# Performance work log

Measured on AMD Instinct MI355X. Metric: run time of the kernel, lower is better.

The kernel has to match this reference:

```python
import jax, jax.numpy as jnp
import numpy as np

B, S, T = 512, 1024, 48  # batch, seq_len, num_tags


def setup_inputs() -> dict:
    key = jax.random.key(0)
    k1, k2, k3, k4, k5, k6 = jax.random.split(key, 6)
    emissions = jax.random.normal(k1, (B, S, T), dtype=jnp.float32)
    tags = jax.random.randint(k2, (B, S), 0, T)
    lengths = jax.random.randint(k3, (B,), 1, S + 1)
    mask = jnp.arange(S)[None, :] < lengths[:, None]  # contiguous prefix mask, bool
    # learned parameters (nn.Parameter zeros init in the module; use small random here)
    start_transitions = 0.01 * jax.random.normal(k4, (T,), dtype=jnp.float32)
    end_transitions = 0.01 * jax.random.normal(k5, (T,), dtype=jnp.float32)
    transitions = 0.01 * jax.random.normal(k6, (T, T), dtype=jnp.float32)
    return {
        "emissions": emissions,
        "tags": tags,
        "mask": mask,
        "start_transitions": start_transitions,
        "end_transitions": end_transitions,
        "transitions": transitions,
    }


def _log_partition(emissions, mask, start_transitions, end_transitions, transitions):
    # score[b, i] = log-sum over paths ending in tag i (note: this repo indexes
    # transitions[i, j] with j = previous tag inside the partition recursion).
    score0 = start_transitions[None, :] + emissions[:, 0]  # (B, T)

    def step(score, xs):
        emit_t, mask_t = xs  # (B, T), (B,)
        # score_t[b, i] = logsumexp_j(score[b, j] + transitions[i, j]) + emit_t[b, i]
        score_t = jax.nn.logsumexp(score[:, None, :] + transitions[None, :, :], axis=2) + emit_t
        score = jnp.where(mask_t[:, None], score_t, score)
        return score, None

    em = jnp.swapaxes(emissions[:, 1:], 0, 1)  # (S-1, B, T)
    mk = jnp.swapaxes(mask[:, 1:], 0, 1)       # (S-1, B)
    score, _ = jax.lax.scan(step, score0, (em, mk))
    return jax.nn.logsumexp(score + end_transitions[None, :], axis=1)  # (B,)


def _score_sentence(emissions, tags, mask, start_transitions, end_transitions, transitions):
    Bb = emissions.shape[0]
    bidx = jnp.arange(Bb)
    maskf = mask.astype(emissions.dtype)
    score = start_transitions[tags[:, 0]] + emissions[bidx, 0, tags[:, 0]]  # (B,)
    trans_sc = transitions[tags[:, :-1], tags[:, 1:]]  # (B, S-1)
    emit_sc = jnp.take_along_axis(emissions, tags[:, :, None], axis=2)[..., 0]  # (B, S)
    score = score + jnp.sum((trans_sc + emit_sc[:, 1:]) * maskf[:, 1:], axis=1)
    last_idx = jnp.sum(mask.astype(jnp.int32), axis=1) - 1  # (B,)
    last_tags = jnp.take_along_axis(tags, last_idx[:, None], axis=1)[:, 0]
    return score + end_transitions[last_tags]


def reference(emissions, tags, mask, start_transitions, end_transitions, transitions):
    log_denominator = _log_partition(emissions, mask, start_transitions, end_transitions, transitions)
    log_numerator = _score_sentence(emissions, tags, mask, start_transitions, end_transitions, transitions)
    return jnp.mean(log_denominator - log_numerator)
```

## Files before the change

### kernel.cpp

```cpp
#include <hip/hip_runtime.h>

#define BB 512
#define SS 1024
#define TT 48
#define GG 16
#define CK 8
#define NSLOT 5

typedef __attribute__((ext_vector_type(8))) short short8;
typedef __attribute__((ext_vector_type(4))) float float4v;
typedef unsigned uint2v __attribute__((ext_vector_type(2)));

__device__ __forceinline__ unsigned short f2bf(float x) {
    unsigned u = __float_as_uint(x);
    u += 0x7FFFu + ((u >> 16) & 1u);
    return (unsigned short)(u >> 16);
}
__device__ __forceinline__ unsigned pk2bf(float lo, float hi) {
#if __has_builtin(__builtin_amdgcn_cvt_pk_bf16_f32)
    typedef __bf16 bf16x2 __attribute__((ext_vector_type(2)));
    union { bf16x2 v; unsigned u; } cv;
    cv.v = __builtin_amdgcn_cvt_pk_bf16_f32(lo, hi);
    return cv.u;
#else
    return __builtin_amdgcn_perm(__float_as_uint(hi) + 0x8000u,
                                 __float_as_uint(lo) + 0x8000u, 0x07060302u);
#endif
}
__device__ __forceinline__ float bflo(unsigned u) { return __uint_as_float(u << 16); }
__device__ __forceinline__ float bfhi(unsigned u) { return __uint_as_float(u & 0xFFFF0000u); }
__device__ __forceinline__ float wave_sum(float v) {
#pragma unroll
    for (int off = 32; off >= 1; off >>= 1) v += __shfl_xor(v, off, 64);
    return v;
}
__device__ __forceinline__ int wave_sum_i(int v) {
#pragma unroll
    for (int off = 32; off >= 1; off >>= 1) v += __shfl_xor(v, off, 64);
    return v;
}
__device__ __forceinline__ float xgrp_max(float m) {
#if __has_builtin(__builtin_amdgcn_permlane16_swap) && __has_builtin(__builtin_amdgcn_permlane32_swap)
    uint2v a = __builtin_amdgcn_permlane16_swap(__float_as_uint(m), __float_as_uint(m), false, false);
    m = fmaxf(__uint_as_float(a[0]), __uint_as_float(a[1]));
    uint2v b = __builtin_amdgcn_permlane32_swap(__float_as_uint(m), __float_as_uint(m), false, false);
    m = fmaxf(__uint_as_float(b[0]), __uint_as_float(b[1]));
#else
    m = fmaxf(m, __shfl_xor(m, 16, 64));
    m = fmaxf(m, __shfl_xor(m, 32, 64));
#endif
    return m;
}
__device__ __forceinline__ float xgrp_sum(float m) {
#if __has_builtin(__builtin_amdgcn_permlane16_swap) && __has_builtin(__builtin_amdgcn_permlane32_swap)
    uint2v a = __builtin_amdgcn_permlane16_swap(__float_as_uint(m), __float_as_uint(m), false, false);
    m = __uint_as_float(a[0]) + __uint_as_float(a[1]);
    uint2v b = __builtin_amdgcn_permlane32_swap(__float_as_uint(m), __float_as_uint(m), false, false);
    m = __uint_as_float(b[0]) + __uint_as_float(b[1]);
#else
    m += __shfl_xor(m, 16, 64);
    m += __shfl_xor(m, 32, 64);
#endif
    return m;
}

__global__ __launch_bounds__(256)
void crf_numer(const float* __restrict__ em, const int* __restrict__ tags,
               const int* __restrict__ mask, const float* __restrict__ start_tr,
               const float* __restrict__ end_tr, const float* __restrict__ trans,
               float* __restrict__ numer, int* __restrict__ lenArr) {
    const int b = blockIdx.x, tid = threadIdx.x;
    const float* emb = em + (size_t)b * SS * TT;
    const int* tg = tags + (size_t)b * SS;
    const int* mk = mask + (size_t)b * SS;
    const int s0 = tid * 4;
    const int4 t4 = *(const int4*)(tg + s0);
    const int4 m4 = *(const int4*)(mk + s0);
    const int tprev = (tid == 0) ? 0 : tg[s0 - 1];
    int cnt = (m4.x != 0) + (m4.y != 0) + (m4.z != 0) + (m4.w != 0);
    float ns = 0.f;
    if (tid > 0 && m4.x) ns += trans[tprev * TT + t4.x] + emb[(size_t)s0 * TT + t4.x];
    if (m4.y) ns += trans[t4.x * TT + t4.y] + emb[(size_t)(s0 + 1) * TT + t4.y];
    if (m4.z) ns += trans[t4.y * TT + t4.z] + emb[(size_t)(s0 + 2) * TT + t4.z];
    if (m4.w) ns += trans[t4.z * TT + t4.w] + emb[(size_t)(s0 + 3) * TT + t4.w];
    float wsum = wave_sum(ns);
    int wcnt = wave_sum_i(cnt);
    __shared__ float sf[4]; __shared__ int si[4];
    if ((tid & 63) == 0) { sf[tid >> 6] = wsum; si[tid >> 6] = wcnt; }
    __syncthreads();
    if (tid == 0) {
        float tot = sf[0] + sf[1] + sf[2] + sf[3];
        int L = si[0] + si[1] + si[2] + si[3];
        int t0 = tg[0];
        tot += start_tr[t0] + emb[t0] + end_tr[tg[L - 1]];
        numer[b] = tot;
        lenArr[b] = L;
    }
}

__global__ __launch_bounds__(320, 1)
void crf_fwd(const float* __restrict__ em, const float* __restrict__ start_tr,
             const float* __restrict__ end_tr, const float* __restrict__ trans,
             const int* __restrict__ lenArr, float* __restrict__ denomArr) {
    __shared__ uint2 ring[NSLOT * CK * 3 * 64];

    const int tid = threadIdx.x;
    const int wave = tid >> 6, lane = tid & 63;
    const int wgbase = blockIdx.x * GG;

    if (wave == 0) {
        __builtin_amdgcn_s_setprio(1);
        const int n = lane & 15, q = lane >> 4;
        const int bb = wgbase + n;

        short8 afr[3][2];
#pragma unroll
        for (int mt = 0; mt < 3; ++mt) {
            const int so = mt * 16 + n;
#pragma unroll
            for (int kt = 0; kt < 2; ++kt) {
                short8 a;
#pragma unroll
                for (int i = 0; i < 8; ++i) {
                    int si_;
                    if (kt == 0) si_ = (i < 4) ? (q * 4 + i) : (16 + q * 4 + (i - 4));
                    else         si_ = (i < 4) ? (32 + q * 4 + i) : -1;
                    a[i] = (si_ >= 0) ? (short)f2bf(__expf(trans[so * TT + si_])) : (short)0;
                }
                afr[mt][kt] = a;
            }
        }

        const float* em0 = em + (size_t)bb * SS * TT + q * 4;
        float p[3][4];
#pragma unroll
        for (int mt = 0; mt < 3; ++mt) {
            float4 v = *(const float4*)(em0 + mt * 16);
            int sb = mt * 16 + q * 4;
            p[mt][0] = __expf(start_tr[sb + 0] + v.x);
            p[mt][1] = __expf(start_tr[sb + 1] + v.y);
            p[mt][2] = __expf(start_tr[sb + 2] + v.z);
            p[mt][3] = __expf(start_tr[sb + 3] + v.w);
        }

        const int len = lenArr[bb];
        int Lmax = len;
#pragma unroll
        for (int off = 1; off < 64; off <<= 1) {
            int o = __shfl_xor(Lmax, off, 64);
            Lmax = Lmax > o ? Lmax : o;
        }
        const int P = (Lmax + 6) >> 3;

        float dc[3][4];
#pragma unroll
        for (int mt = 0; mt < 3; ++mt)
#pragma unroll
            for (int r = 0; r < 4; ++r) dc[mt][r] = 0.f;
        float lcap = 0.f, logscale = 0.f;
        const float4v Z = {0.f, 0.f, 0.f, 0.f};

        for (int pp = -3; pp < P; ++pp) {
            if (pp >= 0) {
                const uint2* rp = &ring[(pp % NSLOT) * (CK * 3 * 64) + lane];
                uint2 c0 = rp[0], c1 = rp[64], c2v = rp[128];
#pragma unroll
                for (int u = 0; u < 8; ++u) {
                    union { short8 v; unsigned w[4]; } B0, B1;
                    B0.w[0] = pk2bf(p[0][0], p[0][1]); B0.w[1] = pk2bf(p[0][2], p[0][3]);
                    B0.w[2] = pk2bf(p[1][0], p[1][1]); B0.w[3] = pk2bf(p[1][2], p[1][3]);
                    B1.w[0] = pk2bf(p[2][0], p[2][1]); B1.w[1] = pk2bf(p[2][2], p[2][3]);
                    B1.w[2] = 0u; B1.w[3] = 0u;
                    float4v A0a = __builtin_amdgcn_mfma_f32_16x16x32_bf16(afr[0][0], B0.v, Z, 0, 0, 0);
                    float4v A1a = __builtin_amdgcn_mfma_f32_16x16x32_bf16(afr[1][0], B0.v, Z, 0, 0, 0);
                    float4v A2a = __builtin_amdgcn_mfma_f32_16x16x32_bf16(afr[2][0], B0.v, Z, 0, 0, 0);
                    float4v A0b = __builtin_amdgcn_mfma_f32_16x16x32_bf16(afr[0][1], B1.v, Z, 0, 0, 0);
                    float4v A1b = __builtin_amdgcn_mfma_f32_16x16x32_bf16(afr[1][1], B1.v, Z, 0, 0, 0);
                    float4v A2b = __builtin_amdgcn_mfma_f32_16x16x32_bf16(afr[2][1], B1.v, Z, 0, 0, 0);
                    uint2 n0, n1, n2;
                    if (u < 7) {
                        n0 = rp[(u + 1) * 192];
                        n1 = rp[(u + 1) * 192 + 64];
                        n2 = rp[(u + 1) * 192 + 128];
                    }
                    float e00 = bflo(c0.x),  e01 = bfhi(c0.x),  e02 = bflo(c0.y),  e03 = bfhi(c0.y);
                    float e10 = bflo(c1.x),  e11 = bfhi(c1.x),  e12 = bflo(c1.y),  e13 = bfhi(c1.y);
                    float e20 = bflo(c2v.x), e21 = bfhi(c2v.x), e22 = bflo(c2v.y), e23 = bfhi(c2v.y);
                    bool cc = (len == 8 * pp + u + 1);
#pragma unroll
                    for (int mt = 0; mt < 3; ++mt)
#pragma unroll
                        for (int r = 0; r < 4; ++r) dc[mt][r] = cc ? p[mt][r] : dc[mt][r];
                    lcap = cc ? logscale : lcap;
                    p[0][0] = (A0a[0] + A0b[0]) * e00; p[0][1] = (A0a[1] + A0b[1]) * e01;
                    p[0][2] = (A0a[2] + A0b[2]) * e02; p[0][3] = (A0a[3] + A0b[3]) * e03;
                    p[1][0] = (A1a[0] + A1b[0]) * e10; p[1][1] = (A1a[1] + A1b[1]) * e11;
                    p[1][2] = (A1a[2] + A1b[2]) * e12; p[1][3] = (A1a[3] + A1b[3]) * e13;
                    p[2][0] = (A2a[0] + A2b[0]) * e20; p[2][1] = (A2a[1] + A2b[1]) * e21;
                    p[2][2] = (A2a[2] + A2b[2]) * e22; p[2][3] = (A2a[3] + A2b[3]) * e23;
                    c0 = n0; c1 = n1; c2v = n2;
                    if (u == 7) {
                        float m = fmaxf(fmaxf(p[0][0], p[0][1]), fmaxf(p[0][2], p[0][3]));
                        m = fmaxf(m, fmaxf(fmaxf(p[1][0], p[1][1]), fmaxf(p[1][2], p[1][3])));
                        m = fmaxf(m, fmaxf(fmaxf(p[2][0], p[2][1]), fmaxf(p[2][2], p[2][3])));
                        m = xgrp_max(m);
                        m = fmaxf(m, 1e-30f);
                        logscale += __logf(m);
                        float rm = __builtin_amdgcn_rcpf(m);
#pragma unroll
                        for (int mt = 0; mt < 3; ++mt)
#pragma unroll
                            for (int r = 0; r < 4; ++r) p[mt][r] *= rm;
                    }
                }
            }
            __builtin_amdgcn_s_barrier();
        }
        {
            bool cc = (len == 8 * P + 1);
#pragma unroll
            for (int mt = 0; mt < 3; ++mt)
#pragma unroll
                for (int r = 0; r < 4; ++r) dc[mt][r] = cc ? p[mt][r] : dc[mt][r];
            lcap = cc ? logscale : lcap;
        }

        float pe = 0.f;
#pragma unroll
        for (int mt = 0; mt < 3; ++mt) {
            int sb = mt * 16 + q * 4;
            pe = fmaf(dc[mt][0], __expf(end_tr[sb + 0]), pe);
            pe = fmaf(dc[mt][1], __expf(end_tr[sb + 1]), pe);
            pe = fmaf(dc[mt][2], __expf(end_tr[sb + 2]), pe);
            pe = fmaf(dc[mt][3], __expf(end_tr[sb + 3]), pe);
        }
        pe = xgrp_sum(pe);
        if (lane < 16) denomArr[bb] = lcap + __logf(pe);

    } else {
        const int T = (wave - 1) >> 1;
        const int sub = (wave - 1) & 1;
        const int nb = lane & 15, q4 = lane >> 4;
        const int bb = wgbase + nb;
        const int len_v = lenArr[bb];
        int Lmax = len_v;
#pragma unroll
        for (int off = 1; off < 64; off <<= 1) {
            int o = __shfl_xor(Lmax, off, 64);
            Lmax = Lmax > o ? Lmax : o;
        }
        const int P = (Lmax + 6) >> 3;

        const float* emP = em + (size_t)bb * SS * TT + q4 * 4;
        float4 buf[12];

        for (int pp = -3; pp < P; ++pp) {
            int cv = pp + 1;
            if (cv >= 0 && cv < P && (cv & 1) == T) {
                uint2* wp = &ring[(cv % NSLOT) * (CK * 3 * 64) + lane];
#pragma unroll
                for (int k = 0; k < 12; ++k) {
                    const int i = sub * 12 + k, u = i / 3, j = i % 3;
                    int t = 1 + 8 * cv + u;
                    bool live = t < len_v;
                    float4 v = buf[k];
                    unsigned ox = pk2bf(__expf(v.x), __expf(v.y));
                    unsigned oy = pk2bf(__expf(v.z), __expf(v.w));
                    uint2 o;
                    o.x = live ? ox : 0u;
                    o.y = live ? oy : 0u;
                    wp[u * 192 + j * 64] = o;
                }
            }
            int ci = pp + 3;
            if (ci < P && (ci & 1) == T) {
#pragma unroll
                for (int k = 0; k < 12; ++k) {
                    const int i = sub * 12 + k, u = i / 3, j = i % 3;
                    int t = 1 + 8 * ci + u; t = t < SS ? t : SS - 1;
                    buf[k] = *(const float4*)(emP + (size_t)t * TT + j * 16);
                }
            }
            __builtin_amdgcn_s_waitcnt(0xC07F);
            __builtin_amdgcn_s_barrier();
        }
    }
}

__global__ __launch_bounds__(64)
void crf_reduce(const float* __restrict__ denom, const float* __restrict__ numer,
                float* __restrict__ out) {
    int lane = threadIdx.x;
    float s = 0.f;
    for (int i = lane; i < BB; i += 64) s += denom[i] - numer[i];
    s = wave_sum(s);
    if (lane == 0) out[0] = s * (1.0f / (float)BB);
}

extern "C" void kernel_launch(void* const* d_in, const int* in_sizes, int n_in,
                              void* d_out, int out_size, void* d_ws, size_t ws_size,
                              hipStream_t stream) {
    const float* emissions = (const float*)d_in[0];
    const int*   tags      = (const int*)d_in[1];
    const int*   mask      = (const int*)d_in[2];
    const float* start_tr  = (const float*)d_in[3];
    const float* end_tr    = (const float*)d_in[4];
    const float* trans     = (const float*)d_in[5];

    char* ws = (char*)d_ws;
    float* denom = (float*)ws;
    float* numer = (float*)(ws + 2048);
    int*   lenA  = (int*)(ws + 4096);

    crf_numer<<<BB, 256, 0, stream>>>(emissions, tags, mask, start_tr, end_tr,
                                      trans, numer, lenA);
    crf_fwd<<<BB / GG, 320, 0, stream>>>(emissions, start_tr, end_tr, trans,
                                         lenA, denom);
    crf_reduce<<<1, 64, 0, stream>>>(denom, numer, (float*)d_out);
}
```

Measured before the change: 339.0 us.

## Interleave two 16-sequence batches per compute wave and store fp32 emission ring

Each workgroup now handles 32 sequences. The MFMA wave runs two independent forward recursions, A and B, interleaving their MFMAs to hide dependency latency, and chains the two K-halves through the accumulator instead of adding them afterwards. The LDS ring now holds fp32 exp(emissions) instead of bf16, which removes the unpack work. Producer waves drop from four to three, staggered over three chunks, and the capture bookkeeping is skipped unless a ballot says some sequence ends in that chunk. Halving the grid to 16 workgroups cuts GPU-wide parallelism, and fp32 staging doubles LDS traffic.

```diff
diff --git a/kernel.cpp b/kernel.cpp
--- a/kernel.cpp
+++ b/kernel.cpp
@@ -3,9 +3,9 @@
 #define BB 512
 #define SS 1024
 #define TT 48
-#define GG 16
+#define GG 32
 #define CK 8
-#define NSLOT 5
+#define NSLOT 3
 
 typedef __attribute__((ext_vector_type(8))) short short8;
 typedef __attribute__((ext_vector_type(4))) float float4v;
@@ -27,8 +27,6 @@
                                  __float_as_uint(lo) + 0x8000u, 0x07060302u);
 #endif
 }
-__device__ __forceinline__ float bflo(unsigned u) { return __uint_as_float(u << 16); }
-__device__ __forceinline__ float bfhi(unsigned u) { return __uint_as_float(u & 0xFFFF0000u); }
 __device__ __forceinline__ float wave_sum(float v) {
 #pragma unroll
     for (int off = 32; off >= 1; off >>= 1) v += __shfl_xor(v, off, 64);
@@ -98,20 +96,21 @@
     }
 }
 
-__global__ __launch_bounds__(320, 1)
+__global__ __launch_bounds__(256, 1)
 void crf_fwd(const float* __restrict__ em, const float* __restrict__ start_tr,
              const float* __restrict__ end_tr, const float* __restrict__ trans,
              const int* __restrict__ lenArr, float* __restrict__ denomArr) {
-    __shared__ uint2 ring[NSLOT * CK * 3 * 64];
+    __shared__ float4v ring[NSLOT * CK * 3 * 2 * 64];
 
     const int tid = threadIdx.x;
     const int wave = tid >> 6, lane = tid & 63;
     const int wgbase = blockIdx.x * GG;
+    const float4v Zv = {0.f, 0.f, 0.f, 0.f};
 
     if (wave == 0) {
         __builtin_amdgcn_s_setprio(1);
         const int n = lane & 15, q = lane >> 4;
-        const int bb = wgbase + n;
+        const int bbA = wgbase + n, bbB = wgbase + 16 + n;
 
         short8 afr[3][2];
 #pragma unroll
@@ -131,20 +130,24 @@
             }
         }
 
-        const float* em0 = em + (size_t)bb * SS * TT + q * 4;
-        float p[3][4];
+        const float* em0A = em + (size_t)bbA * SS * TT + q * 4;
+        const float* em0B = em + (size_t)bbB * SS * TT + q * 4;
+        float4v pA[3], pB[3];
 #pragma unroll
         for (int mt = 0; mt < 3; ++mt) {
-            float4 v = *(const float4*)(em0 + mt * 16);
-            int sb = mt * 16 + q * 4;
-            p[mt][0] = __expf(start_tr[sb + 0] + v.x);
-            p[mt][1] = __expf(start_tr[sb + 1] + v.y);
-            p[mt][2] = __expf(start_tr[sb + 2] + v.z);
-            p[mt][3] = __expf(start_tr[sb + 3] + v.w);
-        }
-
-        const int len = lenArr[bb];
-        int Lmax = len;
+            float4v vA = *(const float4v*)(em0A + mt * 16);
+            float4v vB = *(const float4v*)(em0B + mt * 16);
+            const int sb = mt * 16 + q * 4;
+#pragma unroll
+            for (int r = 0; r < 4; ++r) {
+                float st = start_tr[sb + r];
+                pA[mt][r] = __expf(st + vA[r]);
+                pB[mt][r] = __expf(st + vB[r]);
+            }
+        }
+
+        const int lenA = lenArr[bbA], lenB = lenArr[bbB];
+        int Lmax = lenA > lenB ? lenA : lenB;
 #pragma unroll
         for (int off = 1; off < 64; off <<= 1) {
             int o = __shfl_xor(Lmax, off, 64);
@@ -152,98 +155,115 @@
         }
         const int P = (Lmax + 6) >> 3;
 
-        float dc[3][4];
-#pragma unroll
-        for (int mt = 0; mt < 3; ++mt)
-#pragma unroll
-            for (int r = 0; r < 4; ++r) dc[mt][r] = 0.f;
-        float lcap = 0.f, logscale = 0.f;
-        const float4v Z = {0.f, 0.f, 0.f, 0.f};
+        float4v dcA[3], dcB[3];
+        {
+            const bool c0A = (lenA == 1), c0B = (lenB == 1);
+#pragma unroll
+            for (int mt = 0; mt < 3; ++mt) {
+                dcA[mt] = c0A ? pA[mt] : Zv;
+                dcB[mt] = c0B ? pB[mt] : Zv;
+            }
+        }
+        float lcapA = 0.f, lcapB = 0.f, lsA = 0.f, lsB = 0.f;
 
         for (int pp = -3; pp < P; ++pp) {
             if (pp >= 0) {
-                const uint2* rp = &ring[(pp % NSLOT) * (CK * 3 * 64) + lane];
-                uint2 c0 = rp[0], c1 = rp[64], c2v = rp[128];
+                const float4v* rp = ring + (size_t)(pp % NSLOT) * (CK * 3 * 2 * 64) + lane;
+                float4v cA0 = rp[0],  cA1 = rp[128], cA2 = rp[256];
+                float4v cB0 = rp[64], cB1 = rp[192], cB2 = rp[320];
+                const int lo = 8 * pp + 2, hi = 8 * pp + 9;
+                const bool any =
+                    __ballot(((lenA >= lo) & (lenA <= hi)) | ((lenB >= lo) & (lenB <= hi))) != 0ull;
 #pragma unroll
                 for (int u = 0; u < 8; ++u) {
-                    union { short8 v; unsigned w[4]; } B0, B1;
-                    B0.w[0] = pk2bf(p[0][0], p[0][1]); B0.w[1] = pk2bf(p[0][2], p[0][3]);
-                    B0.w[2] = pk2bf(p[1][0], p[1][1]); B0.w[3] = pk2bf(p[1][2], p[1][3]);
-                    B1.w[0] = pk2bf(p[2][0], p[2][1]); B1.w[1] = pk2bf(p[2][2], p[2][3]);
-                    B1.w[2] = 0u; B1.w[3] = 0u;
-                    float4v A0a = __builtin_amdgcn_mfma_f32_16x16x32_bf16(afr[0][0], B0.v, Z, 0, 0, 0);
-                    float4v A1a = __builtin_amdgcn_mfma_f32_16x16x32_bf16(afr[1][0], B0.v, Z, 0, 0, 0);
-                    float4v A2a = __builtin_amdgcn_mfma_f32_16x16x32_bf16(afr[2][0], B0.v, Z, 0, 0, 0);
-                    float4v A0b = __builtin_amdgcn_mfma_f32_16x16x32_bf16(afr[0][1], B1.v, Z, 0, 0, 0);
-                    float4v A1b = __builtin_amdgcn_mfma_f32_16x16x32_bf16(afr[1][1], B1.v, Z, 0, 0, 0);
-                    float4v A2b = __builtin_amdgcn_mfma_f32_16x16x32_bf16(afr[2][1], B1.v, Z, 0, 0, 0);
-                    uint2 n0, n1, n2;
+                    union { short8 v; unsigned w[4]; } BA0, BA1, BB0, BB1;
+                    BA0.w[0] = pk2bf(pA[0][0], pA[0][1]); BA0.w[1] = pk2bf(pA[0][2], pA[0][3]);
+                    BA0.w[2] = pk2bf(pA[1][0], pA[1][1]); BA0.w[3] = pk2bf(pA[1][2], pA[1][3]);
+                    BA1.w[0] = pk2bf(pA[2][0], pA[2][1]); BA1.w[1] = pk2bf(pA[2][2], pA[2][3]);
+                    BA1.w[2] = 0u; BA1.w[3] = 0u;
+                    BB0.w[0] = pk2bf(pB[0][0], pB[0][1]); BB0.w[1] = pk2bf(pB[0][2], pB[0][3]);
+                    BB0.w[2] = pk2bf(pB[1][0], pB[1][1]); BB0.w[3] = pk2bf(pB[1][2], pB[1][3]);
+                    BB1.w[0] = pk2bf(pB[2][0], pB[2][1]); BB1.w[1] = pk2bf(pB[2][2], pB[2][3]);
+                    BB1.w[2] = 0u; BB1.w[3] = 0u;
+                    float4v rA0 = __builtin_amdgcn_mfma_f32_16x16x32_bf16(afr[0][0], BA0.v, Zv, 0, 0, 0);
+                    float4v rB0 = __builtin_amdgcn_mfma_f32_16x16x32_bf16(afr[0][0], BB0.v, Zv, 0, 0, 0);
+                    float4v rA1 = __builtin_amdgcn_mfma_f32_16x16x32_bf16(afr[1][0], BA0.v, Zv, 0, 0, 0);
+                    float4v rB1 = __builtin_amdgcn_mfma_f32_16x16x32_bf16(afr[1][0], BB0.v, Zv, 0, 0, 0);
+                    float4v rA2 = __builtin_amdgcn_mfma_f32_16x16x32_bf16(afr[2][0], BA0.v, Zv, 0, 0, 0);
+                    float4v rB2 = __builtin_amdgcn_mfma_f32_16x16x32_bf16(afr[2][0], BB0.v, Zv, 0, 0, 0);
+                    rA0 = __builtin_amdgcn_mfma_f32_16x16x32_bf16(afr[0][1], BA1.v, rA0, 0, 0, 0);
+                    rB0 = __builtin_amdgcn_mfma_f32_16x16x32_bf16(afr[0][1], BB1.v, rB0, 0, 0, 0);
+                    rA1 = __builtin_amdgcn_mfma_f32_16x16x32_bf16(afr[1][1], BA1.v, rA1, 0, 0, 0);
+                    rB1 = __builtin_amdgcn_mfma_f32_16x16x32_bf16(afr[1][1], BB1.v, rB1, 0, 0, 0);
+                    rA2 = __builtin_amdgcn_mfma_f32_16x16x32_bf16(afr[2][1], BA1.v, rA2, 0, 0, 0);
+                    rB2 = __builtin_amdgcn_mfma_f32_16x16x32_bf16(afr[2][1], BB1.v, rB2, 0, 0, 0);
+                    float4v nA0, nA1, nA2, nB0, nB1, nB2;
                     if (u < 7) {
-                        n0 = rp[(u + 1) * 192];
-                        n1 = rp[(u + 1) * 192 + 64];
-                        n2 = rp[(u + 1) * 192 + 128];
+                        nA0 = rp[(u + 1) * 384];       nA1 = rp[(u + 1) * 384 + 128];
+                        nA2 = rp[(u + 1) * 384 + 256];
+                        nB0 = rp[(u + 1) * 384 + 64];  nB1 = rp[(u + 1) * 384 + 192];
+                        nB2 = rp[(u + 1) * 384 + 320];
                     }
-                    float e00 = bflo(c0.x),  e01 = bfhi(c0.x),  e02 = bflo(c0.y),  e03 = bfhi(c0.y);
-                    float e10 = bflo(c1.x),  e11 = bfhi(c1.x),  e12 = bflo(c1.y),  e13 = bfhi(c1.y);
-                    float e20 = bflo(c2v.x), e21 = bfhi(c2v.x), e22 = bflo(c2v.y), e23 = bfhi(c2v.y);
-                    bool cc = (len == 8 * pp + u + 1);
-#pragma unroll
-                    for (int mt = 0; mt < 3; ++mt)
-#pragma unroll
-                        for (int r = 0; r < 4; ++r) dc[mt][r] = cc ? p[mt][r] : dc[mt][r];
-                    lcap = cc ? logscale : lcap;
-                    p[0][0] = (A0a[0] + A0b[0]) * e00; p[0][1] = (A0a[1] + A0b[1]) * e01;
-                    p[0][2] = (A0a[2] + A0b[2]) * e02; p[0][3] = (A0a[3] + A0b[3]) * e03;
-                    p[1][0] = (A1a[0] + A1b[0]) * e10; p[1][1] = (A1a[1] + A1b[1]) * e11;
-                    p[1][2] = (A1a[2] + A1b[2]) * e12; p[1][3] = (A1a[3] + A1b[3]) * e13;
-                    p[2][0] = (A2a[0] + A2b[0]) * e20; p[2][1] = (A2a[1] + A2b[1]) * e21;
-                    p[2][2] = (A2a[2] + A2b[2]) * e22; p[2][3] = (A2a[3] + A2b[3]) * e23;
-                    c0 = n0; c1 = n1; c2v = n2;
+                    pA[0] = rA0 * cA0; pA[1] = rA1 * cA1; pA[2] = rA2 * cA2;
+                    pB[0] = rB0 * cB0; pB[1] = rB1 * cB1; pB[2] = rB2 * cB2;
+                    if (any) {
+                        const bool ccA = (lenA == 8 * pp + u + 2);
+                        const bool ccB = (lenB == 8 * pp + u + 2);
+#pragma unroll
+                        for (int mt = 0; mt < 3; ++mt) {
+                            dcA[mt] = ccA ? pA[mt] : dcA[mt];
+                            dcB[mt] = ccB ? pB[mt] : dcB[mt];
+                        }
+                        lcapA = ccA ? lsA : lcapA;
+                        lcapB = ccB ? lsB : lcapB;
+                    }
+                    cA0 = nA0; cA1 = nA1; cA2 = nA2;
+                    cB0 = nB0; cB1 = nB1; cB2 = nB2;
                     if (u == 7) {
-                        float m = fmaxf(fmaxf(p[0][0], p[0][1]), fmaxf(p[0][2], p[0][3]));
-                        m = fmaxf(m, fmaxf(fmaxf(p[1][0], p[1][1]), fmaxf(p[1][2], p[1][3])));
-                        m = fmaxf(m, fmaxf(fmaxf(p[2][0], p[2][1]), fmaxf(p[2][2], p[2][3])));
-                        m = xgrp_max(m);
-                        m = fmaxf(m, 1e-30f);
-                        logscale += __logf(m);
-                        float rm = __builtin_amdgcn_rcpf(m);
-#pragma unroll
-                        for (int mt = 0; mt < 3; ++mt)
-#pragma unroll
-                            for (int r = 0; r < 4; ++r) p[mt][r] *= rm;
+                        float mA = fmaxf(fmaxf(pA[0][0], pA[0][1]), fmaxf(pA[0][2], pA[0][3]));
+                        mA = fmaxf(mA, fmaxf(fmaxf(pA[1][0], pA[1][1]), fmaxf(pA[1][2], pA[1][3])));
+                        mA = fmaxf(mA, fmaxf(fmaxf(pA[2][0], pA[2][1]), fmaxf(pA[2][2], pA[2][3])));
+                        float mB = fmaxf(fmaxf(pB[0][0], pB[0][1]), fmaxf(pB[0][2], pB[0][3]));
+                        mB = fmaxf(mB, fmaxf(fmaxf(pB[1][0], pB[1][1]), fmaxf(pB[1][2], pB[1][3])));
+                        mB = fmaxf(mB, fmaxf(fmaxf(pB[2][0], pB[2][1]), fmaxf(pB[2][2], pB[2][3])));
+                        mA = fmaxf(xgrp_max(mA), 1e-30f);
+                        mB = fmaxf(xgrp_max(mB), 1e-30f);
+                        lsA += __logf(mA);
+                        lsB += __logf(mB);
+                        const float rmA = __builtin_amdgcn_rcpf(mA);
+                        const float rmB = __builtin_amdgcn_rcpf(mB);
+                        pA[0] *= rmA; pA[1] *= rmA; pA[2] *= rmA;
+                        pB[0] *= rmB; pB[1] *= rmB; pB[2] *= rmB;
                     }
                 }
             }
             __builtin_amdgcn_s_barrier();
         }
-        {
-            bool cc = (len == 8 * P + 1);
-#pragma unroll
-            for (int mt = 0; mt < 3; ++mt)
-#pragma unroll
-                for (int r = 0; r < 4; ++r) dc[mt][r] = cc ? p[mt][r] : dc[mt][r];
-            lcap = cc ? logscale : lcap;
-        }
-
-        float pe = 0.f;
+
+        float peA = 0.f, peB = 0.f;
 #pragma unroll
         for (int mt = 0; mt < 3; ++mt) {
-            int sb = mt * 16 + q * 4;
-            pe = fmaf(dc[mt][0], __expf(end_tr[sb + 0]), pe);
-            pe = fmaf(dc[mt][1], __expf(end_tr[sb + 1]), pe);
-            pe = fmaf(dc[mt][2], __expf(end_tr[sb + 2]), pe);
-            pe = fmaf(dc[mt][3], __expf(end_tr[sb + 3]), pe);
-        }
-        pe = xgrp_sum(pe);
-        if (lane < 16) denomArr[bb] = lcap + __logf(pe);
+            const int sb = mt * 16 + q * 4;
+#pragma unroll
+            for (int r = 0; r < 4; ++r) {
+                float ee = __expf(end_tr[sb + r]);
+                peA = fmaf(dcA[mt][r], ee, peA);
+                peB = fmaf(dcB[mt][r], ee, peB);
+            }
+        }
+        peA = xgrp_sum(peA);
+        peB = xgrp_sum(peB);
+        if (lane < 16) {
+            denomArr[bbA] = lcapA + __logf(peA);
+            denomArr[bbB] = lcapB + __logf(peB);
+        }
 
     } else {
-        const int T = (wave - 1) >> 1;
-        const int sub = (wave - 1) & 1;
+        const int w = wave - 1;
         const int nb = lane & 15, q4 = lane >> 4;
-        const int bb = wgbase + nb;
-        const int len_v = lenArr[bb];
-        int Lmax = len_v;
+        const int bbA = wgbase + nb, bbB = wgbase + 16 + nb;
+        const int lenA_v = lenArr[bbA], lenB_v = lenArr[bbB];
+        int Lmax = lenA_v > lenB_v ? lenA_v : lenB_v;
 #pragma unroll
         for (int off = 1; off < 64; off <<= 1) {
             int o = __shfl_xor(Lmax, off, 64);
@@ -251,34 +271,54 @@
         }
         const int P = (Lmax + 6) >> 3;
 
-        const float* emP = em + (size_t)bb * SS * TT + q4 * 4;
-        float4 buf[12];
+        const float* emA = em + (size_t)bbA * SS * TT + q4 * 4;
+        const float* emB = em + (size_t)bbB * SS * TT + q4 * 4;
+        float4v buf[24];
 
         for (int pp = -3; pp < P; ++pp) {
-            int cv = pp + 1;
-            if (cv >= 0 && cv < P && (cv & 1) == T) {
-                uint2* wp = &ring[(cv % NSLOT) * (CK * 3 * 64) + lane];
-#pragma unroll
-                for (int k = 0; k < 12; ++k) {
-                    const int i = sub * 12 + k, u = i / 3, j = i % 3;
-                    int t = 1 + 8 * cv + u;
-                    bool live = t < len_v;
-                    float4 v = buf[k];
-                    unsigned ox = pk2bf(__expf(v.x), __expf(v.y));
-                    unsigned oy = pk2bf(__expf(v.z), __expf(v.w));
-                    uint2 o;
-                    o.x = live ? ox : 0u;
-                    o.y = live ? oy : 0u;
-                    wp[u * 192 + j * 64] = o;
-                }
-            }
-            int ci = pp + 3;
-            if (ci < P && (ci & 1) == T) {
-#pragma unroll
-                for (int k = 0; k < 12; ++k) {
-                    const int i = sub * 12 + k, u = i / 3, j = i % 3;
+            const int ci = pp + 3;
+            if (ci < P && ci % 3 == w) {
+#pragma unroll
+                for (int kk = 0; kk < 24; ++kk) {
+                    const int u = kk / 3, j = kk % 3;
                     int t = 1 + 8 * ci + u; t = t < SS ? t : SS - 1;
-                    buf[k] = *(const float4*)(emP + (size_t)t * TT + j * 16);
+                    buf[kk] = *(const float4v*)(emA + (size_t)t * TT + j * 16);
+                }
+            }
+            const int ca = pp + 2;
+            if (ca >= 0 && ca < P && ca % 3 == w) {
+                float4v* wp = ring + (size_t)(ca % NSLOT) * (CK * 3 * 2 * 64) + lane;
+#pragma unroll
+                for (int kk = 0; kk < 24; ++kk) {
+                    const int u = kk / 3, j = kk % 3;
+                    const int t = 1 + 8 * ca + u;
+                    float4v v = buf[kk];
+                    float4v o;
+                    o[0] = __expf(v[0]); o[1] = __expf(v[1]);
+                    o[2] = __expf(v[2]); o[3] = __expf(v[3]);
+                    o = (t < lenA_v) ? o : Zv;
+                    wp[(size_t)(u * 3 + j) * 128] = o;
+                }
+#pragma unroll
+                for (int kk = 0; kk < 24; ++kk) {
+                    const int u = kk / 3, j = kk % 3;
+                    int t = 1 + 8 * ca + u; t = t < SS ? t : SS - 1;
+                    buf[kk] = *(const float4v*)(emB + (size_t)t * TT + j * 16);
+                }
+            }
+            const int cb = pp + 1;
+            if (cb >= 0 && cb < P && cb % 3 == w) {
+                float4v* wp = ring + (size_t)(cb % NSLOT) * (CK * 3 * 2 * 64) + 64 + lane;
+#pragma unroll
+                for (int kk = 0; kk < 24; ++kk) {
+                    const int u = kk / 3, j = kk % 3;
+                    const int t = 1 + 8 * cb + u;
+                    float4v v = buf[kk];
+                    float4v o;
+                    o[0] = __expf(v[0]); o[1] = __expf(v[1]);
+                    o[2] = __expf(v[2]); o[3] = __expf(v[3]);
+                    o = (t < lenB_v) ? o : Zv;
+                    wp[(size_t)(u * 3 + j) * 128] = o;
                 }
             }
             __builtin_amdgcn_s_waitcnt(0xC07F);
@@ -314,7 +354,7 @@
 
     crf_numer<<<BB, 256, 0, stream>>>(emissions, tags, mask, start_tr, end_tr,
                                       trans, numer, lenA);
-    crf_fwd<<<BB / GG, 320, 0, stream>>>(emissions, start_tr, end_tr, trans,
+    crf_fwd<<<BB / GG, 256, 0, stream>>>(emissions, start_tr, end_tr, trans,
                                          lenA, denom);
     crf_reduce<<<1, 64, 0, stream>>>(denom, numer, (float*)d_out);
 }
```

Result: slower. 430.2 us (+26.9%).
